# Kernel optimization log

Measured on AMD Instinct MI355X. Metric: run time of the kernel, lower is better.

The kernel has to match this reference:

```python
import jax, jax.numpy as jnp
import numpy as np

CODEBOOK_SIZE = 8192
DIM = 256
COMMITMENT_COST = 0.25


def setup_inputs() -> dict:
    key = jax.random.key(0)
    k1, k2 = jax.random.split(key)
    z = jax.random.normal(k1, (8, DIM, 1024), dtype=jnp.float32)
    # nn.init.uniform_(codebook.weight, -1/K, 1/K)
    bound = 1.0 / CODEBOOK_SIZE
    codebook = jax.random.uniform(k2, (CODEBOOK_SIZE, DIM), dtype=jnp.float32,
                                  minval=-bound, maxval=bound)
    return {"z": z, "codebook": codebook}


def reference(z, codebook):
    B, D, T = z.shape
    z_perm = jnp.transpose(z, (0, 2, 1)).reshape(B * T, D)  # (BT, D)
    # ||z||^2 - 2 z.c + ||c||^2  -> (BT, K)
    distances = (jnp.sum(z_perm * z_perm, axis=1, keepdims=True)
                 - 2.0 * (z_perm @ codebook.T)
                 + jnp.sum(codebook * codebook, axis=1)[None, :])
    indices = jnp.argmin(distances, axis=1)          # (BT,)
    z_q_flat = codebook[indices]                     # (BT, D)
    z_q = jnp.transpose(z_q_flat.reshape(B, T, D), (0, 2, 1))  # (B, D, T)

    codebook_loss = jnp.mean((z_q - jax.lax.stop_gradient(z)) ** 2)
    commitment_loss = COMMITMENT_COST * jnp.mean((jax.lax.stop_gradient(z_q) - z) ** 2)
    loss = codebook_loss + commitment_loss

    # straight-through estimator
    z_q_st = z + jax.lax.stop_gradient(z_q - z)
    return z_q_st, indices.reshape(B, T), loss
```

## Files before the change

kernel.cpp:

```cpp
#include <hip/hip_runtime.h>

#define DD   256
#define TT   1024
#define BT   8192
#define KK   8192
#define ZQ_SIZE 2097152

#define FLT_INF 3.402823466e38f

typedef __attribute__((ext_vector_type(8))) short short8;
typedef __attribute__((ext_vector_type(4))) float f32x4;

#define ASP_B   0u
#define BSP_B   12582912u
#define AN_B    25165824u
#define CN_B    25198592u
#define KEY_B   25231360u
#define ACC_B   25296896u

static __device__ __forceinline__ unsigned short f2bf(float x) {
    unsigned int u = __float_as_uint(x);
    return (unsigned short)((u + 0x7FFF + ((u >> 16) & 1)) >> 16);
}
static __device__ __forceinline__ float bf2f(unsigned short h) {
    return __uint_as_float(((unsigned int)h) << 16);
}
static __device__ __forceinline__ void split3(float x, unsigned short& h,
                                              unsigned short& m, unsigned short& l) {
    h = f2bf(x);
    float r1 = x - bf2f(h);
    m = f2bf(r1);
    l = f2bf(r1 - bf2f(m));
}

static __device__ __forceinline__ void gld16(const void* g, const void* l) {
    __builtin_amdgcn_global_load_lds(
        (const __attribute__((address_space(1))) unsigned int*)g,
        (__attribute__((address_space(3))) unsigned int*)l, 16, 0, 0);
}

__global__ __launch_bounds__(256) void vq_prep(const float* __restrict__ z,
                                               const float* __restrict__ cb,
                                               float* __restrict__ An,
                                               unsigned short* __restrict__ Asp,
                                               unsigned short* __restrict__ Bsp,
                                               float* __restrict__ Cn,
                                               unsigned long long* __restrict__ keys,
                                               float* __restrict__ lacc) {
    __shared__ float T[64][257];
    int tid = threadIdx.x;
    if (blockIdx.x < 32) {
        int g = blockIdx.x * 256 + tid;
        int b = g >> 10, t = g & 1023;
        const float* zp = z + (size_t)b * (DD * TT) + t;
        float s = 0.f;
        #pragma unroll 8
        for (int d = 0; d < DD; ++d) {
            float v = zp[d * TT];
            float v2 = v * v;
            s = s + v2;
        }
        An[g] = s;
        keys[g] = ~0ull;
        if (g == 0) *lacc = 0.f;
    } else if (blockIdx.x < 32 + 2048) {
        int g = (blockIdx.x - 32) * 256 + tid;
        int code = g >> 6, d4 = (g & 63) * 4;
        float4 v = *(const float4*)&cb[(size_t)code * DD + d4];
        unsigned short h[4], m[4], l[4];
        split3(v.x, h[0], m[0], l[0]);
        split3(v.y, h[1], m[1], l[1]);
        split3(v.z, h[2], m[2], l[2]);
        split3(v.w, h[3], m[3], l[3]);
        unsigned short* row = Bsp + (size_t)code * 768 + d4;
        *(ushort4*)&row[0]   = make_ushort4(h[0], h[1], h[2], h[3]);
        *(ushort4*)&row[256] = make_ushort4(m[0], m[1], m[2], m[3]);
        *(ushort4*)&row[512] = make_ushort4(l[0], l[1], l[2], l[3]);
        float s = v.x * v.x + v.y * v.y + v.z * v.z + v.w * v.w;
        #pragma unroll
        for (int off = 32; off; off >>= 1) s += __shfl_down(s, off, 64);
        if ((tid & 63) == 0) Cn[code] = s;
    } else {
        int blk = blockIdx.x - 2080;
        int b = blk >> 4;
        int t0 = (blk & 15) * 64;
        #pragma unroll
        for (int it = 0; it < 16; ++it) {
            int d = it * 16 + (tid >> 4);
            int t4 = (tid & 15) * 4;
            float4 v = *(const float4*)&z[(size_t)b * (DD * TT) + (size_t)d * TT + t0 + t4];
            T[t4 + 0][d] = v.x; T[t4 + 1][d] = v.y; T[t4 + 2][d] = v.z; T[t4 + 3][d] = v.w;
        }
        __syncthreads();
        int r = tid >> 2, q = tid & 3;
        int token = b * 1024 + t0 + r;
        unsigned short* arow = Asp + (size_t)token * 768;
        #pragma unroll
        for (int dd = 0; dd < 16; ++dd) {
            int d = dd * 16 + q * 4;
            unsigned short h[4], m[4], l[4];
            #pragma unroll
            for (int c = 0; c < 4; ++c) split3(T[r][d + c], h[c], m[c], l[c]);
            *(ushort4*)&arow[d]       = make_ushort4(h[0], h[1], h[2], h[3]);
            *(ushort4*)&arow[256 + d] = make_ushort4(m[0], m[1], m[2], m[3]);
            *(ushort4*)&arow[512 + d] = make_ushort4(l[0], l[1], l[2], l[3]);
        }
    }
}

__global__ __launch_bounds__(256, 2) void vq_scores(const unsigned short* __restrict__ Asp,
                                                    const unsigned short* __restrict__ Bsp,
                                                    const float* __restrict__ An,
                                                    const float* __restrict__ Cn,
                                                    unsigned long long* __restrict__ keys) {
    __shared__ __attribute__((aligned(16))) unsigned short Abuf[2][8192];
    __shared__ __attribute__((aligned(16))) unsigned short Bbuf[2][12288];

    int bid = blockIdx.x;
    int g = bid >> 6, sl = bid & 63;
    int mt = (g >> 3) * 8 + (sl >> 3);
    int nt = (g & 7) * 8 + (sl & 7);
    const int token0 = mt * 256, code0 = nt * 128;

    const int wid = threadIdx.x >> 6, lane = threadIdx.x & 63;
    const int m0w = wid * 64;

    const int srl = lane >> 2;
    const int sq  = lane & 3;
    const int fs  = (((sq + (srl >> 2)) & 3) ^ (srl & 3));
    const size_t arow = (size_t)(token0 + wid * 64 + srl) * 768 + fs * 8;
    const size_t brow = (size_t)(code0 + srl) * 768 + fs * 8;
    const int albase = (wid * 64) * 32;

    f32x4 acc[4][8];
    #pragma unroll
    for (int i = 0; i < 4; ++i)
        #pragma unroll
        for (int j = 0; j < 8; ++j) acc[i][j] = (f32x4){0.f, 0.f, 0.f, 0.f};

    #pragma unroll
    for (int n = 0; n < 6; ++n) {
        int grp = wid * 6 + n;
        int part = grp >> 3, rb = (grp & 7) * 16;
        gld16(Bsp + brow + (size_t)rb * 768 + part * 256,
              &Bbuf[0][part * 4096 + rb * 32]);
    }
    #pragma unroll
    for (int n = 0; n < 4; ++n)
        gld16(Asp + arow + (size_t)(n * 16) * 768, &Abuf[0][albase + n * 16 * 32]);

    const int quad = lane >> 4, col = lane & 15;
    const int qp = ((quad ^ (col & 3)) - (col >> 2)) & 3;

    for (int kk = 0; kk < 8; ++kk) {
        #pragma unroll
        for (int ph = 0; ph < 3; ++ph) {
            __syncthreads();
            if (ph == 0) {
                #pragma unroll
                for (int n = 0; n < 4; ++n)
                    gld16(Asp + arow + (size_t)(n * 16) * 768 + 256 + kk * 32,
                          &Abuf[(kk + 1) & 1][albase + n * 16 * 32]);
            } else if (ph == 1) {
                #pragma unroll
                for (int n = 0; n < 4; ++n)
                    gld16(Asp + arow + (size_t)(n * 16) * 768 + 512 + kk * 32,
                          &Abuf[kk & 1][albase + n * 16 * 32]);
            } else if (kk < 7) {
                #pragma unroll
                for (int n = 0; n < 6; ++n) {
                    int grp = wid * 6 + n;
                    int part = grp >> 3, rb = (grp & 7) * 16;
                    gld16(Bsp + brow + (size_t)rb * 768 + part * 256 + (kk + 1) * 32,
                          &Bbuf[(kk + 1) & 1][part * 4096 + rb * 32]);
                }
                #pragma unroll
                for (int n = 0; n < 4; ++n)
                    gld16(Asp + arow + (size_t)(n * 16) * 768 + (kk + 1) * 32,
                          &Abuf[(kk + 1) & 1][albase + n * 16 * 32]);
            }

            const unsigned short* A = Abuf[(kk + ph) & 1];
            const unsigned short* B = Bbuf[kk & 1];

            short8 af[4];
            #pragma unroll
            for (int i = 0; i < 4; ++i)
                af[i] = *(const short8*)&A[(m0w + i * 16 + col) * 32 + qp * 8];

            const int nparts = 3 - ph;
            for (int bp = 0; bp < nparts; ++bp) {
                short8 bf[8];
                #pragma unroll
                for (int j = 0; j < 8; ++j)
                    bf[j] = *(const short8*)&B[bp * 4096 + (j * 16 + col) * 32 + qp * 8];
                #pragma unroll
                for (int i = 0; i < 4; ++i)
                    #pragma unroll
                    for (int j = 0; j < 8; ++j)
                        acc[i][j] = __builtin_amdgcn_mfma_f32_16x16x32_bf16(
                            af[i], bf[j], acc[i][j], 0, 0, 0);
            }
        }
    }

    float cn[8]; int cidx[8];
    #pragma unroll
    for (int j = 0; j < 8; ++j) {
        cidx[j] = code0 + j * 16 + col;
        cn[j] = Cn[cidx[j]];
    }
    #pragma unroll
    for (int i = 0; i < 4; ++i) {
        #pragma unroll
        for (int r = 0; r < 4; ++r) {
            int token = token0 + m0w + i * 16 + quad * 4 + r;
            float Ai = An[token];
            float bv = FLT_INF; int bi = 0;
            #pragma unroll
            for (int j = 0; j < 8; ++j) {
                float d1 = fmaf(-2.f, acc[i][j][r], Ai);
                float dist = d1 + cn[j];
                if (dist < bv) { bv = dist; bi = cidx[j]; }
            }
            #pragma unroll
            for (int off = 8; off; off >>= 1) {
                float ov = __shfl_down(bv, off, 16);
                int   oi = __shfl_down(bi, off, 16);
                if (ov < bv || (ov == bv && oi < bi)) { bv = ov; bi = oi; }
            }
            if (col == 0) {
                unsigned long long key =
                    ((unsigned long long)__float_as_uint(bv) << 32) | (unsigned)bi;
                atomicMin(&keys[token], key);
            }
        }
    }
}

__global__ __launch_bounds__(256) void vq_gather(const float* __restrict__ z,
                                                 const float* __restrict__ cb,
                                                 const unsigned long long* __restrict__ keys,
                                                 float* __restrict__ out,
                                                 float* __restrict__ out_idx,
                                                 float* __restrict__ loss_acc) {
    int e4 = blockIdx.x * 256 + threadIdx.x;
    int t4 = e4 & 255;
    int rest = e4 >> 8;
    int d = rest & 255;
    int b = rest >> 8;
    int gbase = b * 1024 + t4 * 4;

    const int* klo = (const int*)keys;
    int i0 = klo[(size_t)(gbase + 0) * 2];
    int i1 = klo[(size_t)(gbase + 1) * 2];
    int i2 = klo[(size_t)(gbase + 2) * 2];
    int i3 = klo[(size_t)(gbase + 3) * 2];
    if (d == 0) {
        out_idx[gbase + 0] = (float)i0;
        out_idx[gbase + 1] = (float)i1;
        out_idx[gbase + 2] = (float)i2;
        out_idx[gbase + 3] = (float)i3;
    }

    float4 zv = *(const float4*)&z[(size_t)e4 * 4];
    float q0 = cb[(size_t)i0 * DD + d];
    float q1 = cb[(size_t)i1 * DD + d];
    float q2 = cb[(size_t)i2 * DD + d];
    float q3 = cb[(size_t)i3 * DD + d];

    float d0 = q0 - zv.x, d1 = q1 - zv.y, d2 = q2 - zv.z, d3 = q3 - zv.w;
    float4 o;
    o.x = zv.x + d0; o.y = zv.y + d1; o.z = zv.z + d2; o.w = zv.w + d3;
    *(float4*)&out[(size_t)e4 * 4] = o;

    float s = d0 * d0 + d1 * d1 + d2 * d2 + d3 * d3;
    #pragma unroll
    for (int off = 32; off; off >>= 1) s += __shfl_down(s, off, 64);
    __shared__ float wsum[4];
    if ((threadIdx.x & 63) == 0) wsum[threadIdx.x >> 6] = s;
    __syncthreads();
    if (threadIdx.x == 0)
        atomicAdd(loss_acc, wsum[0] + wsum[1] + wsum[2] + wsum[3]);
}

__global__ void vq_loss(const float* __restrict__ loss_acc, float* __restrict__ out_loss) {
    *out_loss = 1.25f * (*loss_acc) / 2097152.f;
}

extern "C" void kernel_launch(void* const* d_in, const int* in_sizes, int n_in,
                              void* d_out, int out_size, void* d_ws, size_t ws_size,
                              hipStream_t stream) {
    const float* z  = (const float*)d_in[0];
    const float* cb = (const float*)d_in[1];
    float* out = (float*)d_out;
    char*  w   = (char*)d_ws;

    unsigned short* Asp = (unsigned short*)(w + ASP_B);
    unsigned short* Bsp = (unsigned short*)(w + BSP_B);
    float* An = (float*)(w + AN_B);
    float* Cn = (float*)(w + CN_B);
    unsigned long long* keys = (unsigned long long*)(w + KEY_B);
    float* lacc = (float*)(w + ACC_B);

    vq_prep   <<<32 + 2048 + 128, 256, 0, stream>>>(z, cb, An, Asp, Bsp, Cn, keys, lacc);
    vq_scores <<<2048, 256, 0, stream>>>(Asp, Bsp, An, Cn, keys);
    vq_gather <<<ZQ_SIZE / 1024, 256, 0, stream>>>(z, cb, keys, out, out + ZQ_SIZE, lacc);
    vq_loss   <<<1, 1, 0, stream>>>(lacc, out + ZQ_SIZE + BT);
}
```

Measured before the change: 298.5 us.

## Pre-swizzle split-bf16 operands into MFMA fragment layout, load A directly from global

```diff
diff --git a/kernel.cpp b/kernel.cpp
--- a/kernel.cpp
+++ b/kernel.cpp
@@ -11,8 +11,8 @@
 typedef __attribute__((ext_vector_type(8))) short short8;
 typedef __attribute__((ext_vector_type(4))) float f32x4;
 
-#define ASP_B   0u
-#define BSP_B   12582912u
+#define A2_B    0u
+#define B2_B    12582912u
 #define AN_B    25165824u
 #define CN_B    25198592u
 #define KEY_B   25231360u
@@ -42,8 +42,8 @@
 __global__ __launch_bounds__(256) void vq_prep(const float* __restrict__ z,
                                                const float* __restrict__ cb,
                                                float* __restrict__ An,
-                                               unsigned short* __restrict__ Asp,
-                                               unsigned short* __restrict__ Bsp,
+                                               unsigned short* __restrict__ A2,
+                                               unsigned short* __restrict__ B2,
                                                float* __restrict__ Cn,
                                                unsigned long long* __restrict__ keys,
                                                float* __restrict__ lacc) {
@@ -72,10 +72,14 @@
         split3(v.y, h[1], m[1], l[1]);
         split3(v.z, h[2], m[2], l[2]);
         split3(v.w, h[3], m[3], l[3]);
-        unsigned short* row = Bsp + (size_t)code * 768 + d4;
-        *(ushort4*)&row[0]   = make_ushort4(h[0], h[1], h[2], h[3]);
-        *(ushort4*)&row[256] = make_ushort4(m[0], m[1], m[2], m[3]);
-        *(ushort4*)&row[512] = make_ushort4(l[0], l[1], l[2], l[3]);
+        int ng = code >> 4;
+        int lane = ((d4 >> 3) & 3) * 16 + (code & 15);
+        int kk = d4 >> 5;
+        int jb = d4 & 7;
+        size_t base = (size_t)((ng * 3) * 8 + kk) * 512 + lane * 8 + jb;
+        *(ushort4*)&B2[base]        = make_ushort4(h[0], h[1], h[2], h[3]);
+        *(ushort4*)&B2[base + 4096] = make_ushort4(m[0], m[1], m[2], m[3]);
+        *(ushort4*)&B2[base + 8192] = make_ushort4(l[0], l[1], l[2], l[3]);
         float s = v.x * v.x + v.y * v.y + v.z * v.z + v.w * v.w;
         #pragma unroll
         for (int off = 32; off; off >>= 1) s += __shfl_down(s, off, 64);
@@ -93,28 +97,29 @@
         }
         __syncthreads();
         int r = tid >> 2, q = tid & 3;
-        int token = b * 1024 + t0 + r;
-        unsigned short* arow = Asp + (size_t)token * 768;
+        int t = b * 1024 + t0 + r;
+        int gA = t >> 4, ml = t & 15;
         #pragma unroll
         for (int dd = 0; dd < 16; ++dd) {
             int d = dd * 16 + q * 4;
             unsigned short h[4], m[4], l[4];
             #pragma unroll
             for (int c = 0; c < 4; ++c) split3(T[r][d + c], h[c], m[c], l[c]);
-            *(ushort4*)&arow[d]       = make_ushort4(h[0], h[1], h[2], h[3]);
-            *(ushort4*)&arow[256 + d] = make_ushort4(m[0], m[1], m[2], m[3]);
-            *(ushort4*)&arow[512 + d] = make_ushort4(l[0], l[1], l[2], l[3]);
-        }
-    }
-}
-
-__global__ __launch_bounds__(256, 2) void vq_scores(const unsigned short* __restrict__ Asp,
-                                                    const unsigned short* __restrict__ Bsp,
+            int kk = d >> 5, quad = (d >> 3) & 3, jb = d & 7;
+            size_t base = (size_t)((gA * 3) * 8 + kk) * 512 + (quad * 16 + ml) * 8 + jb;
+            *(ushort4*)&A2[base]        = make_ushort4(h[0], h[1], h[2], h[3]);
+            *(ushort4*)&A2[base + 4096] = make_ushort4(m[0], m[1], m[2], m[3]);
+            *(ushort4*)&A2[base + 8192] = make_ushort4(l[0], l[1], l[2], l[3]);
+        }
+    }
+}
+
+__global__ __launch_bounds__(256, 2) void vq_scores(const unsigned short* __restrict__ A2,
+                                                    const unsigned short* __restrict__ B2,
                                                     const float* __restrict__ An,
                                                     const float* __restrict__ Cn,
                                                     unsigned long long* __restrict__ keys) {
-    __shared__ __attribute__((aligned(16))) unsigned short Abuf[2][8192];
-    __shared__ __attribute__((aligned(16))) unsigned short Bbuf[2][12288];
+    __shared__ __attribute__((aligned(16))) unsigned short Bl[2][12288];
 
     int bid = blockIdx.x;
     int g = bid >> 6, sl = bid & 63;
@@ -123,14 +128,16 @@
     const int token0 = mt * 256, code0 = nt * 128;
 
     const int wid = threadIdx.x >> 6, lane = threadIdx.x & 63;
-    const int m0w = wid * 64;
-
-    const int srl = lane >> 2;
-    const int sq  = lane & 3;
-    const int fs  = (((sq + (srl >> 2)) & 3) ^ (srl & 3));
-    const size_t arow = (size_t)(token0 + wid * 64 + srl) * 768 + fs * 8;
-    const size_t brow = (size_t)(code0 + srl) * 768 + fs * 8;
-    const int albase = (wid * 64) * 32;
+    const int quad = lane >> 4, col = lane & 15;
+
+    int sidx[6]; size_t soff[6];
+    #pragma unroll
+    for (int n = 0; n < 6; ++n) {
+        int idx = wid * 6 + n;
+        int p = idx >> 3, ngl = idx & 7;
+        sidx[n] = idx * 512;
+        soff[n] = (size_t)(((nt * 8 + ngl) * 3 + p) * 8) * 512 + lane * 8;
+    }
 
     f32x4 acc[4][8];
     #pragma unroll
@@ -139,68 +146,41 @@
         for (int j = 0; j < 8; ++j) acc[i][j] = (f32x4){0.f, 0.f, 0.f, 0.f};
 
     #pragma unroll
-    for (int n = 0; n < 6; ++n) {
-        int grp = wid * 6 + n;
-        int part = grp >> 3, rb = (grp & 7) * 16;
-        gld16(Bsp + brow + (size_t)rb * 768 + part * 256,
-              &Bbuf[0][part * 4096 + rb * 32]);
-    }
-    #pragma unroll
-    for (int n = 0; n < 4; ++n)
-        gld16(Asp + arow + (size_t)(n * 16) * 768, &Abuf[0][albase + n * 16 * 32]);
-
-    const int quad = lane >> 4, col = lane & 15;
-    const int qp = ((quad ^ (col & 3)) - (col >> 2)) & 3;
+    for (int n = 0; n < 6; ++n)
+        gld16(B2 + soff[n], &Bl[0][sidx[n]]);
+
+    const int gm0 = (token0 >> 4) + wid * 4;
+    const int PP[6] = {0, 1, 2, 0, 1, 0};
+    const int QQ[6] = {0, 0, 0, 1, 1, 2};
 
     for (int kk = 0; kk < 8; ++kk) {
-        #pragma unroll
-        for (int ph = 0; ph < 3; ++ph) {
-            __syncthreads();
-            if (ph == 0) {
-                #pragma unroll
-                for (int n = 0; n < 4; ++n)
-                    gld16(Asp + arow + (size_t)(n * 16) * 768 + 256 + kk * 32,
-                          &Abuf[(kk + 1) & 1][albase + n * 16 * 32]);
-            } else if (ph == 1) {
-                #pragma unroll
-                for (int n = 0; n < 4; ++n)
-                    gld16(Asp + arow + (size_t)(n * 16) * 768 + 512 + kk * 32,
-                          &Abuf[kk & 1][albase + n * 16 * 32]);
-            } else if (kk < 7) {
-                #pragma unroll
-                for (int n = 0; n < 6; ++n) {
-                    int grp = wid * 6 + n;
-                    int part = grp >> 3, rb = (grp & 7) * 16;
-                    gld16(Bsp + brow + (size_t)rb * 768 + part * 256 + (kk + 1) * 32,
-                          &Bbuf[(kk + 1) & 1][part * 4096 + rb * 32]);
-                }
-                #pragma unroll
-                for (int n = 0; n < 4; ++n)
-                    gld16(Asp + arow + (size_t)(n * 16) * 768 + (kk + 1) * 32,
-                          &Abuf[(kk + 1) & 1][albase + n * 16 * 32]);
-            }
-
-            const unsigned short* A = Abuf[(kk + ph) & 1];
-            const unsigned short* B = Bbuf[kk & 1];
-
-            short8 af[4];
-            #pragma unroll
-            for (int i = 0; i < 4; ++i)
-                af[i] = *(const short8*)&A[(m0w + i * 16 + col) * 32 + qp * 8];
-
-            const int nparts = 3 - ph;
-            for (int bp = 0; bp < nparts; ++bp) {
-                short8 bf[8];
+        __syncthreads();
+        if (kk < 7) {
+            #pragma unroll
+            for (int n = 0; n < 6; ++n)
+                gld16(B2 + soff[n] + (size_t)(kk + 1) * 512, &Bl[(kk + 1) & 1][sidx[n]]);
+        }
+        const unsigned short* B = Bl[kk & 1];
+        short8 bf[8];
+        #pragma unroll
+        for (int t = 0; t < 6; ++t) {
+            const int p = PP[t], q = QQ[t];
+            if (t == 0 || q != QQ[t - 1]) {
                 #pragma unroll
                 for (int j = 0; j < 8; ++j)
-                    bf[j] = *(const short8*)&B[bp * 4096 + (j * 16 + col) * 32 + qp * 8];
+                    bf[j] = *(const short8*)&B[(q * 8 + j) * 512 + lane * 8];
+            }
+            short8 af[4];
+            #pragma unroll
+            for (int i = 0; i < 4; ++i)
+                af[i] = *(const short8*)&A2[(size_t)(((gm0 + i) * 3 + p) * 8 + kk) * 512
+                                            + lane * 8];
+            #pragma unroll
+            for (int i = 0; i < 4; ++i)
                 #pragma unroll
-                for (int i = 0; i < 4; ++i)
-                    #pragma unroll
-                    for (int j = 0; j < 8; ++j)
-                        acc[i][j] = __builtin_amdgcn_mfma_f32_16x16x32_bf16(
-                            af[i], bf[j], acc[i][j], 0, 0, 0);
-            }
+                for (int j = 0; j < 8; ++j)
+                    acc[i][j] = __builtin_amdgcn_mfma_f32_16x16x32_bf16(
+                        af[i], bf[j], acc[i][j], 0, 0, 0);
         }
     }
 
@@ -214,7 +194,7 @@
     for (int i = 0; i < 4; ++i) {
         #pragma unroll
         for (int r = 0; r < 4; ++r) {
-            int token = token0 + m0w + i * 16 + quad * 4 + r;
+            int token = token0 + wid * 64 + i * 16 + quad * 4 + r;
             float Ai = An[token];
             float bv = FLT_INF; int bi = 0;
             #pragma unroll
@@ -296,15 +276,15 @@
     float* out = (float*)d_out;
     char*  w   = (char*)d_ws;
 
-    unsigned short* Asp = (unsigned short*)(w + ASP_B);
-    unsigned short* Bsp = (unsigned short*)(w + BSP_B);
+    unsigned short* A2 = (unsigned short*)(w + A2_B);
+    unsigned short* B2 = (unsigned short*)(w + B2_B);
     float* An = (float*)(w + AN_B);
     float* Cn = (float*)(w + CN_B);
     unsigned long long* keys = (unsigned long long*)(w + KEY_B);
     float* lacc = (float*)(w + ACC_B);
 
-    vq_prep   <<<32 + 2048 + 128, 256, 0, stream>>>(z, cb, An, Asp, Bsp, Cn, keys, lacc);
-    vq_scores <<<2048, 256, 0, stream>>>(Asp, Bsp, An, Cn, keys);
+    vq_prep   <<<32 + 2048 + 128, 256, 0, stream>>>(z, cb, An, A2, B2, Cn, keys, lacc);
+    vq_scores <<<2048, 256, 0, stream>>>(A2, B2, An, Cn, keys);
     vq_gather <<<ZQ_SIZE / 1024, 256, 0, stream>>>(z, cb, keys, out, out + ZQ_SIZE, lacc);
     vq_loss   <<<1, 1, 0, stream>>>(lacc, out + ZQ_SIZE + BT);
 }
```

Measured after the change: 269.2 us. 9.8% less time.
